# Kernel optimization log

Hardware: AMD Instinct MI355X
Metric: run time of the kernel (lower is better)

## Reference

```python
import jax, jax.numpy as jnp
import numpy as np

B, A, GS = 4, 256, 12           # graphs, atoms per graph, grid size
NG = GS ** 3                    # 1728 grid nodes per graph
K_A, K_G = 8, 32                # atom kNN, grid->atom kNN
L, CODE, HID, EDGE = 4, 64, 128, 64
NTYPES, NGAUSS, CUT, SPACING = 16, 20, 5.0, 1.5
N_NODES = B * A + B * NG


def _grid_coords():
    half = (GS - 1) * SPACING / 2.0
    g = jnp.linspace(-half, half, GS)
    mesh = jnp.meshgrid(g, g, g, indexing='ij')
    return jnp.stack(mesh, axis=-1).reshape(-1, 3)  # [NG, 3]


def _gauss_consts():
    # GaussianSmearing(type_='exp', start=0, stop=cutoff, num_gaussians=20)
    off = jnp.exp(jnp.linspace(np.log(1.0), np.log(CUT + 1.0), NGAUSS)) - 1.0
    d = jnp.diff(off)
    d = jnp.concatenate([d[:1], d])
    return off, -0.5 / d ** 2


def _build_edges(pos):
    # pos: [B*A, 3] atom coords, per-graph kNN (batch = 256 atoms per graph)
    atom_pos = pos.reshape(B, A, 3)
    # atom-atom kNN (loop=False): edge (neighbor j -> atom i)
    d2 = jnp.sum((atom_pos[:, :, None, :] - atom_pos[:, None, :, :]) ** 2, -1)
    d2 = d2 + jnp.eye(A) * 1e9  # exclude self loops
    _, nbr = jax.lax.top_k(-d2, K_A)                       # [B, A, K_A]
    src_a = (nbr + (jnp.arange(B) * A)[:, None, None]).reshape(-1)
    dst_a = jnp.repeat(jnp.arange(B * A), K_A)
    # grid->atom kNN: each grid node receives from its K_G nearest atoms
    grid = _grid_coords()
    gd2 = jnp.sum((grid[None, :, None, :] - atom_pos[:, None, :, :]) ** 2, -1)  # [B, NG, A]
    _, gn = jax.lax.top_k(-gd2, K_G)                       # [B, NG, K_G]
    src_g = (gn + (jnp.arange(B) * A)[:, None, None]).reshape(-1)
    dst_g = B * A + jnp.repeat(jnp.arange(B * NG), K_G)
    return jnp.concatenate([src_a, src_g]), jnp.concatenate([dst_a, dst_g])


def _layer(h, node_pos, src, dst, cnt, off, coeff, eW, eb, W1, b1, W2, b2, g, beta):
    rel = node_pos[src] - node_pos[dst]
    dist = jnp.clip(jnp.sqrt(jnp.sum(rel ** 2, -1)), 0.0, CUT)
    gauss = jnp.exp(coeff * (dist[:, None] - off) ** 2)    # [E, 20]
    ef = gauss @ eW + eb                                   # [E, EDGE]
    mi = jnp.concatenate([h[src], h[dst], ef], -1)         # [E, 2*CODE+EDGE]
    m = jax.nn.relu(mi @ W1 + b1) @ W2 + b2                # [E, CODE]
    aggr = jax.ops.segment_sum(m, dst, num_segments=N_NODES) / cnt[:, None]
    x = h + aggr
    mu = jnp.mean(x, -1, keepdims=True)
    var = jnp.var(x, -1, keepdims=True)
    return (x - mu) / jnp.sqrt(var + 1e-5) * g + beta


def setup_inputs() -> dict:
    key = jax.random.key(0)
    ks = jax.random.split(key, 6)
    s = 0.05
    return {
        'pos': jax.random.uniform(ks[0], (B * A, 3), minval=-8.0, maxval=8.0),
        'atom_types': jax.random.randint(ks[1], (B * A,), 0, NTYPES),
        'batch': jnp.repeat(jnp.arange(B), A),
        'edge_W': jax.random.normal(ks[2], (L, NGAUSS, EDGE)) * s,
        'edge_b': jnp.zeros((L, EDGE)),
        'W1': jax.random.normal(ks[3], (L, 2 * CODE + EDGE, HID)) * s,
        'b1': jnp.zeros((L, HID)),
        'W2': jax.random.normal(ks[4], (L, HID, CODE)) * s,
        'b2': jnp.zeros((L, CODE)),
        'ln_g': jnp.ones((L, CODE)),
        'ln_b': jnp.zeros((L, CODE)),
    }


def reference(pos, atom_types, batch, edge_W, edge_b, W1, b1, W2, b2, ln_g, ln_b):
    # node features: one-hot atoms padded to code_dim, zero grid codes
    af = jax.nn.one_hot(atom_types, NTYPES, dtype=jnp.float32)
    af = jnp.pad(af, ((0, 0), (0, CODE - NTYPES)))
    h = jnp.concatenate([af, jnp.zeros((B * NG, CODE), jnp.float32)], 0)
    node_pos = jnp.concatenate([pos, jnp.tile(_grid_coords(), (B, 1))], 0)
    src, dst = _build_edges(pos)
    cnt = jnp.clip(jax.ops.segment_sum(jnp.ones_like(dst, jnp.float32), dst,
                                       num_segments=N_NODES), 1.0)
    off, coeff = _gauss_consts()
    for l in range(L):
        h = _layer(h, node_pos, src, dst, cnt, off, coeff,
                   edge_W[l], edge_b[l], W1[l], b1[l], W2[l], b2[l],
                   ln_g[l], ln_b[l])
    return h[B * A:].reshape(B, NG, CODE)
```

## Files before the change

kernel.cpp:

```cpp
#include <hip/hip_runtime.h>
#include <hip/hip_bf16.h>
#include <math.h>

#define NATOMS 1024
#define NGRID  6912
#define NNODES 7936
#define NG_PER 1728
#define KA 8
#define KG 32
#define CODE 64
#define HID 128
#define NT 1024

typedef __hip_bfloat16 bf16;
typedef unsigned long long u64;
typedef unsigned int u32;

static void* g_buf = nullptr;
__attribute__((constructor)) static void _alloc_ws(){
  if (hipMalloc(&g_buf, (size_t)24 * 1024 * 1024) != hipSuccess) g_buf = nullptr;
}

__device__ __forceinline__ float ldf(const void* p, size_t i, int f32){
  return f32 ? ((const float*)p)[i] : __bfloat162float(((const bf16*)p)[i]);
}

__device__ __forceinline__ int ldt(const void* p, int i, int mode){
  switch(mode){
    case 1:  return ((const int*)p)[2*i];
    case 2:  return (int)((const float*)p)[i];
    case 3:  return (int)__bfloat162float(((const bf16*)p)[i]);
    default: return ((const int*)p)[i];
  }
}

__global__ void k0(const unsigned short* __restrict__ posu,
                   const unsigned short* __restrict__ typu,
                   int* __restrict__ flag, float* __restrict__ offc){
  if (blockIdx.x == 0){
    __shared__ int scnt;
    int t = threadIdx.x;
    if (t == 0) scnt = 0;
    __syncthreads();
    int c = 0;
    for (int q = 0; q < 12; q++){
      unsigned short u = posu[t + 256*q];
      int e = (u >> 7) & 0xFF;
      if (e >= 140) c++;
    }
    atomicAdd(&scnt, c);
    __syncthreads();
    if (t == 0) flag[0] = (scnt > 16) ? 1 : 0;
  } else {
    if (threadIdx.x == 0){
      int oddHigh = 0, evenHigh = 0, quadZero = 1;
      for (int k = 0; k < 16; k++){
        unsigned short o = typu[2*k+1], e = typu[2*k];
        if (o >= 0x3F00 && o <= 0x4200) oddHigh++;
        if (e >= 0x3F00 && e <= 0x4200) evenHigh++;
      }
      for (int k = 0; k < 16; k++) if (typu[4*k+2] != 0) quadZero = 0;
      int mode;
      if (oddHigh >= 8) mode = (evenHigh >= 8) ? 3 : 2;
      else              mode = quadZero ? 1 : 0;
      flag[1] = mode;
    }
    int k = (int)threadIdx.x - 64;
    if (k >= 0 && k < 20){
      double step = log(6.0) / 19.0;
      double offk = exp((double)k * step) - 1.0;
      int km = (k == 0) ? 1 : k;
      double d = (exp((double)km * step) - 1.0) - (exp((double)(km - 1) * step) - 1.0);
      offc[k]      = (float)offk;
      offc[20 + k] = (float)(-0.5 / (d * d));
    }
  }
}

__global__ void __launch_bounds__(256) k_pre(const void* __restrict__ pos,
    const void* __restrict__ types, const int* __restrict__ flag,
    float* __restrict__ node_pos, float* __restrict__ h0,
    int* __restrict__ nbrA, int* __restrict__ nbrG){
  #pragma clang fp contract(off)
  __shared__ __attribute__((aligned(16))) u64 sK[4][256];
  int f32 = flag[0];
  int b = blockIdx.x;
  int t = threadIdx.x;
  if (b < 1984){
    int tm = flag[1];
    int idx = b * 256 + t;
    if (idx < NNODES){
      if (idx < NATOMS){
        node_pos[idx*3+0] = ldf(pos, idx*3+0, f32);
        node_pos[idx*3+1] = ldf(pos, idx*3+1, f32);
        node_pos[idx*3+2] = ldf(pos, idx*3+2, f32);
      } else {
        int cell = (idx - NATOMS) % NG_PER;
        int ix = cell / 144, iy = (cell / 12) % 12, iz = cell % 12;
        node_pos[idx*3+0] = -8.25f + 1.5f * ix;
        node_pos[idx*3+1] = -8.25f + 1.5f * iy;
        node_pos[idx*3+2] = -8.25f + 1.5f * iz;
      }
    }
    int node = idx >> 6, c = idx & 63;
    float v = 0.f;
    if (node < NATOMS && c == ldt(types, node, tm)) v = 1.f;
    h0[idx] = v;
  } else if (b < 1984 + 256){
    int i = (b - 1984) * 4 + (t >> 6);
    int bb = i >> 8, li = i & 255;
    int l = t & 63;
    float px = ldf(pos,3*i,f32), py = ldf(pos,3*i+1,f32), pz = ldf(pos,3*i+2,f32);
    u64 vals[4];
    for (int q = 0; q < 4; q++){
      int c = l + 64*q;
      int j = (bb << 8) + c;
      float dx = ldf(pos,3*j+0,f32) - px;
      float dy = ldf(pos,3*j+1,f32) - py;
      float dz = ldf(pos,3*j+2,f32) - pz;
      float d2 = (dx*dx + dy*dy) + dz*dz;
      vals[q] = (c == li) ? ~0ull : (((u64)__float_as_uint(d2) << 8) | (unsigned)c);
    }
    for (int it = 0; it < KA; it++){
      u64 v = vals[0];
      for (int q = 1; q < 4; q++) if (vals[q] < v) v = vals[q];
      for (int m = 1; m < 64; m <<= 1){
        u64 ov = __shfl_xor(v, m);
        if (ov < v) v = ov;
      }
      int widx = (int)(v & 0xFF);
      if (l == 0) nbrA[i*KA + it] = (bb << 8) + widx;
      if ((widx & 63) == l) vals[widx >> 6] = ~0ull;
    }
  } else {
    int w  = t >> 6;
    int gi = (b - 2240) * 4 + w;
    int bb = gi / NG_PER, cell = gi % NG_PER;
    int ix = cell / 144, iy = (cell / 12) % 12, iz = cell % 12;
    double px = -8.25 + 1.5 * ix;
    double py = -8.25 + 1.5 * iy;
    double pz = -8.25 + 1.5 * iz;
    int l = t & 63;
    u64* sk = &sK[w][0];
    u64 vals[4];
    #pragma unroll
    for (int q = 0; q < 4; q++){
      int c = l + 64*q;
      int j = (bb << 8) + c;
      double dx = px - (double)ldf(pos,3*j+0,f32);
      double dy = py - (double)ldf(pos,3*j+1,f32);
      double dz = pz - (double)ldf(pos,3*j+2,f32);
      double d2 = dx*dx + dy*dy + dz*dz;
      u64 key = ((u64)__double_as_longlong(d2) & ~0xFFull) | (unsigned)c;
      vals[q] = key;
      sk[c] = key;
    }
    __syncthreads();
    int r0 = 0, r1 = 0, r2 = 0, r3 = 0;
    #pragma unroll 4
    for (int j = 0; j < 256; j += 2){
      ulonglong2 kk = *(const ulonglong2*)&sk[j];
      r0 += (kk.x < vals[0]); r0 += (kk.y < vals[0]);
      r1 += (kk.x < vals[1]); r1 += (kk.y < vals[1]);
      r2 += (kk.x < vals[2]); r2 += (kk.y < vals[2]);
      r3 += (kk.x < vals[3]); r3 += (kk.y < vals[3]);
    }
    int base = (bb << 8) + l;
    if (r0 < KG) nbrG[gi*KG + r0] = base;
    if (r1 < KG) nbrG[gi*KG + r1] = base + 64;
    if (r2 < KG) nbrG[gi*KG + r2] = base + 128;
    if (r3 < KG) nbrG[gi*KG + r3] = base + 192;
  }
}

__global__ void __launch_bounds__(128) k_fold(const float* __restrict__ hin,
    const void* __restrict__ W1, const void* __restrict__ b1,
    const void* __restrict__ eW, const void* __restrict__ eb,
    size_t wl, size_t b1o, size_t eWo, size_t ebo,
    const int* __restrict__ flag,
    float* __restrict__ Xd, float* __restrict__ Xs,
    float* __restrict__ Wg, float* __restrict__ b1p,
    const float* __restrict__ offc, float2* __restrict__ Tt)
{
  __shared__ __attribute__((aligned(16))) float sA[1344];
  __shared__ float sB[192];
  int f32 = flag[0];
  int t = threadIdx.x;
  int b = blockIdx.x;
  if (b < 1120){
    int isXd = (b < 992);
    size_t wo = wl + (isXd ? (size_t)64*128 : 0);
    int r0 = (isXd ? b : (b - 992)) * 8;
    float* C = isXd ? Xd : Xs;
    float w[64];
    #pragma unroll
    for (int k = 0; k < 64; k++) w[k] = ldf(W1, wo + (size_t)k*128 + t, f32);
    for (int i = t; i < 8*64; i += 128) sA[i] = hin[(size_t)r0*64 + i];
    __syncthreads();
    #pragma unroll
    for (int r = 0; r < 8; r += 4){
      float a0 = 0.f, a1 = 0.f, a2 = 0.f, a3 = 0.f;
      #pragma unroll
      for (int k4 = 0; k4 < 16; k4++){
        float4 v0 = *(const float4*)&sA[(r+0)*64 + 4*k4];
        float4 v1 = *(const float4*)&sA[(r+1)*64 + 4*k4];
        float4 v2 = *(const float4*)&sA[(r+2)*64 + 4*k4];
        float4 v3 = *(const float4*)&sA[(r+3)*64 + 4*k4];
        a0 = fmaf(v0.x, w[4*k4+0], a0); a0 = fmaf(v0.y, w[4*k4+1], a0);
        a0 = fmaf(v0.z, w[4*k4+2], a0); a0 = fmaf(v0.w, w[4*k4+3], a0);
        a1 = fmaf(v1.x, w[4*k4+0], a1); a1 = fmaf(v1.y, w[4*k4+1], a1);
        a1 = fmaf(v1.z, w[4*k4+2], a1); a1 = fmaf(v1.w, w[4*k4+3], a1);
        a2 = fmaf(v2.x, w[4*k4+0], a2); a2 = fmaf(v2.y, w[4*k4+1], a2);
        a2 = fmaf(v2.z, w[4*k4+2], a2); a2 = fmaf(v2.w, w[4*k4+3], a2);
        a3 = fmaf(v3.x, w[4*k4+0], a3); a3 = fmaf(v3.y, w[4*k4+1], a3);
        a3 = fmaf(v3.z, w[4*k4+2], a3); a3 = fmaf(v3.w, w[4*k4+3], a3);
      }
      C[(size_t)(r0 + r + 0)*128 + t] = a0;
      C[(size_t)(r0 + r + 1)*128 + t] = a1;
      C[(size_t)(r0 + r + 2)*128 + t] = a2;
      C[(size_t)(r0 + r + 3)*128 + t] = a3;
    }
  } else if (b == 1120){
    float w[64];
    #pragma unroll
    for (int k = 0; k < 64; k++) w[k] = ldf(W1, wl + (size_t)128*128 + (size_t)k*128 + t, f32);
    for (int i = t; i < 20*64; i += 128) sA[i] = ldf(eW, eWo + i, f32);
    if (t < 64) sA[1280 + t] = ldf(eb, ebo + t, f32);
    __syncthreads();
    for (int g = 0; g < 20; g++){
      float acc = 0.f;
      #pragma unroll
      for (int k4 = 0; k4 < 16; k4++){
        float4 e = *(const float4*)&sA[g*64 + 4*k4];
        acc = fmaf(e.x, w[4*k4+0], acc); acc = fmaf(e.y, w[4*k4+1], acc);
        acc = fmaf(e.z, w[4*k4+2], acc); acc = fmaf(e.w, w[4*k4+3], acc);
      }
      Wg[g*128 + t] = acc;
    }
    float acc = ldf(b1, b1o + t, f32);
    #pragma unroll
    for (int k4 = 0; k4 < 16; k4++){
      float4 e = *(const float4*)&sA[1280 + 4*k4];
      acc = fmaf(e.x, w[4*k4+0], acc); acc = fmaf(e.y, w[4*k4+1], acc);
      acc = fmaf(e.z, w[4*k4+2], acc); acc = fmaf(e.w, w[4*k4+3], acc);
    }
    b1p[t] = acc;
  } else {
    int r0 = (b - 1121) * 8;
    float w[64];
    #pragma unroll
    for (int k = 0; k < 64; k++) w[k] = ldf(W1, wl + (size_t)128*128 + (size_t)k*128 + t, f32);
    for (int i = t; i < 20*64; i += 128) sA[i] = ldf(eW, eWo + i, f32);
    for (int i = t; i < 180; i += 128){
      int row = i / 20, k = i - row*20;
      float d  = (float)(r0 + row) * (5.0f / (float)NT);
      float dd = d - offc[k];
      sB[i] = expf(offc[20 + k] * dd * dd);
    }
    __syncthreads();
    float wg[20];
    #pragma unroll
    for (int gk = 0; gk < 20; gk++){
      float acc = 0.f;
      #pragma unroll
      for (int k4 = 0; k4 < 16; k4++){
        float4 e = *(const float4*)&sA[gk*64 + 4*k4];
        acc = fmaf(e.x, w[4*k4+0], acc); acc = fmaf(e.y, w[4*k4+1], acc);
        acc = fmaf(e.z, w[4*k4+2], acc); acc = fmaf(e.w, w[4*k4+3], acc);
      }
      wg[gk] = acc;
    }
    float v[9];
    #pragma unroll
    for (int r = 0; r < 9; r++){
      float acc = 0.f;
      #pragma unroll
      for (int k = 0; k < 20; k++) acc = fmaf(sB[r*20 + k], wg[k], acc);
      v[r] = acc;
    }
    #pragma unroll
    for (int r = 0; r < 8; r++)
      Tt[(size_t)(r0 + r)*128 + t] = make_float2(v[r], v[r+1]);
  }
}

__global__ void __launch_bounds__(256) k_aggr(const float* __restrict__ Xs,
    const float* __restrict__ Xd, const int* __restrict__ nbrA,
    const int* __restrict__ nbrG, const float* __restrict__ node_pos,
    const float2* __restrict__ Tt, const float* __restrict__ b1p,
    float* __restrict__ Sbuf)
{
  __shared__ __attribute__((aligned(16))) int   sN[256];
  __shared__ __attribute__((aligned(16))) float sX[256];
  int t = threadIdx.x;
  int b = blockIdx.x;
  int KK, node0; const int* nbr;
  if (b < 32){ KK = 8;  node0 = b*32;              nbr = nbrA + b*256; }
  else       { KK = 32; node0 = NATOMS + (b-32)*8; nbr = nbrG + (size_t)(b-32)*256; }
  {
    int src = nbr[t];
    sN[t] = src;
    int node = node0 + ((b < 32) ? (t >> 3) : (t >> 5));
    float dx = node_pos[src*3+0] - node_pos[node*3+0];
    float dy = node_pos[src*3+1] - node_pos[node*3+1];
    float dz = node_pos[src*3+2] - node_pos[node*3+2];
    float dist = fminf(sqrtf(dx*dx + dy*dy + dz*dz), 5.0f);
    sX[t] = dist * ((float)NT / 5.0f);
  }
  int g = t >> 7, tt = t & 127;
  float b1v = b1p[tt];
  __syncthreads();
  float rK = 1.f / KK;
  int nLoc = (b < 32) ? 16 : 4;
  int nbase = g * nLoc;
  for (int n = 0; n < nLoc; n++){
    int node = node0 + nbase + n;
    float zb = Xd[(size_t)node*128 + tt] + b1v;
    float S = 0.f;
    int ebase = (nbase + n) * KK;
    for (int e = 0; e < KK; e += 4){
      int i0 = ebase + e;
      int4   sv = *(const int4*)&sN[i0];
      float4 xv = *(const float4*)&sX[i0];
      int ia0 = (int)xv.x; if (ia0 > NT-1) ia0 = NT-1;
      int ia1 = (int)xv.y; if (ia1 > NT-1) ia1 = NT-1;
      int ia2 = (int)xv.z; if (ia2 > NT-1) ia2 = NT-1;
      int ia3 = (int)xv.w; if (ia3 > NT-1) ia3 = NT-1;
      float f0 = xv.x - (float)ia0;
      float f1 = xv.y - (float)ia1;
      float f2 = xv.z - (float)ia2;
      float f3 = xv.w - (float)ia3;
      float2 w0 = Tt[(size_t)ia0*128 + tt];
      float2 w1 = Tt[(size_t)ia1*128 + tt];
      float2 w2 = Tt[(size_t)ia2*128 + tt];
      float2 w3 = Tt[(size_t)ia3*128 + tt];
      float a0 = zb + Xs[(size_t)sv.x*128 + tt] + fmaf(f0, w0.y - w0.x, w0.x);
      float a1 = zb + Xs[(size_t)sv.y*128 + tt] + fmaf(f1, w1.y - w1.x, w1.x);
      float a2 = zb + Xs[(size_t)sv.z*128 + tt] + fmaf(f2, w2.y - w2.x, w2.x);
      float a3 = zb + Xs[(size_t)sv.w*128 + tt] + fmaf(f3, w3.y - w3.x, w3.x);
      S += fmaxf(a0,0.f) + fmaxf(a1,0.f) + fmaxf(a2,0.f) + fmaxf(a3,0.f);
    }
    Sbuf[(size_t)node*128 + tt] = S * rK;
  }
}

__global__ void __launch_bounds__(256) k_out(const float* __restrict__ hin,
    const float* __restrict__ Sbuf,
    const void* __restrict__ W2, const void* __restrict__ b2,
    const void* __restrict__ lng, const void* __restrict__ lnb,
    size_t w2o, size_t b2o, size_t lno,
    const int* __restrict__ flag,
    float* __restrict__ hout, float* __restrict__ out, int writeOut)
{
  __shared__ float sW2[128*64];
  __shared__ __attribute__((aligned(16))) float sS[32*128];
  int f32 = flag[0];
  int t = threadIdx.x;
  int r0 = blockIdx.x * 32;
  for (int i = t; i < 128*64; i += 256) sW2[i] = ldf(W2, w2o + i, f32);
  for (int i = t; i < 32*128; i += 256) sS[i] = Sbuf[(size_t)r0*128 + i];
  int w = t >> 6, c = t & 63;
  float b2v = ldf(b2, b2o + c, f32);
  float gv  = ldf(lng, lno + c, f32);
  float bv  = ldf(lnb, lno + c, f32);
  __syncthreads();
  for (int rr = w*8; rr < w*8 + 8; rr += 2){
    float a0 = 0.f, a1 = 0.f;
    const float* s0 = &sS[rr*128];
    const float* s1 = &sS[(rr+1)*128];
    #pragma unroll
    for (int kq = 0; kq < 32; kq++){
      float4 sv0 = *(const float4*)(s0 + 4*kq);
      float4 sv1 = *(const float4*)(s1 + 4*kq);
      a0 = fmaf(sv0.x, sW2[(4*kq+0)*64+c], a0);
      a0 = fmaf(sv0.y, sW2[(4*kq+1)*64+c], a0);
      a0 = fmaf(sv0.z, sW2[(4*kq+2)*64+c], a0);
      a0 = fmaf(sv0.w, sW2[(4*kq+3)*64+c], a0);
      a1 = fmaf(sv1.x, sW2[(4*kq+0)*64+c], a1);
      a1 = fmaf(sv1.y, sW2[(4*kq+1)*64+c], a1);
      a1 = fmaf(sv1.z, sW2[(4*kq+2)*64+c], a1);
      a1 = fmaf(sv1.w, sW2[(4*kq+3)*64+c], a1);
    }
    {
      int node = r0 + rr;
      float x = hin[(size_t)node*64 + c] + a0 + b2v;
      float s = x;
      #pragma unroll
      for (int m = 1; m < 64; m <<= 1) s += __shfl_xor(s, m);
      float mu = s * (1.f/64.f);
      float d = x - mu;
      float v = d * d;
      #pragma unroll
      for (int m = 1; m < 64; m <<= 1) v += __shfl_xor(v, m);
      v *= (1.f/64.f);
      float o = d / sqrtf(v + 1e-5f) * gv + bv;
      hout[(size_t)node*64 + c] = o;
      if (writeOut && node >= NATOMS) out[(size_t)(node - NATOMS)*64 + c] = o;
    }
    {
      int node = r0 + rr + 1;
      float x = hin[(size_t)node*64 + c] + a1 + b2v;
      float s = x;
      #pragma unroll
      for (int m = 1; m < 64; m <<= 1) s += __shfl_xor(s, m);
      float mu = s * (1.f/64.f);
      float d = x - mu;
      float v = d * d;
      #pragma unroll
      for (int m = 1; m < 64; m <<= 1) v += __shfl_xor(v, m);
      v *= (1.f/64.f);
      float o = d / sqrtf(v + 1e-5f) * gv + bv;
      hout[(size_t)node*64 + c] = o;
      if (writeOut && node >= NATOMS) out[(size_t)(node - NATOMS)*64 + c] = o;
    }
  }
}

extern "C" void kernel_launch(void* const* d_in, const int* in_sizes, int n_in,
                              void* d_out, int out_size, void* d_ws, size_t ws_size,
                              hipStream_t stream) {
  const void* pos    = d_in[0];
  const void* types  = d_in[1];
  const void* edge_W = d_in[3];
  const void* edge_b = d_in[4];
  const void* W1     = d_in[5];
  const void* b1     = d_in[6];
  const void* W2     = d_in[7];
  const void* b2     = d_in[8];
  const void* lng    = d_in[9];
  const void* lnb    = d_in[10];

  const size_t NEED = (size_t)16 * 1024 * 1024;
  char* w = (ws_size >= NEED) ? (char*)d_ws : (char*)g_buf;
  if (w == nullptr) w = (char*)d_ws;

  size_t o = 0;
  auto alloc = [&](size_t bytes)->char*{
    char* r = w + o; o = (o + bytes + 255) & ~(size_t)255; return r;
  };
  float*  node_pos = (float*) alloc((size_t)NNODES*3*4);
  float*  hA       = (float*) alloc((size_t)NNODES*CODE*4);
  float*  hB       = (float*) alloc((size_t)NNODES*CODE*4);
  float*  Xs       = (float*) alloc((size_t)NATOMS*HID*4);
  float*  Xd       = (float*) alloc((size_t)NNODES*HID*4);
  float*  Sbuf     = (float*) alloc((size_t)NNODES*HID*4);
  int*    nbrA     = (int*)   alloc((size_t)NATOMS*KA*4);
  int*    nbrG     = (int*)   alloc((size_t)NGRID*KG*4);
  float*  offc     = (float*) alloc(64*4);
  float*  Wg       = (float*) alloc(20*HID*4);
  float*  b1p      = (float*) alloc(HID*4);
  int*    flag     = (int*)   alloc(64*4);
  float2* Tt       = (float2*)alloc((size_t)NT*HID*8);

  k0<<<2, 256, 0, stream>>>((const unsigned short*)pos,
                            (const unsigned short*)types, flag, offc);
  k_pre<<<3968, 256, 0, stream>>>(pos, types, flag, node_pos, hA, nbrA, nbrG);

  float* hin = hA; float* hout = hB;
  for (int l = 0; l < 4; l++){
    size_t wl  = (size_t)l*192*128;
    size_t eWo = (size_t)l*20*64, ebo = (size_t)l*64;
    size_t b1o = (size_t)l*128,   w2o = (size_t)l*128*64;
    size_t b2o = (size_t)l*64,    lno = (size_t)l*64;
    k_fold<<<1121 + 128, 128, 0, stream>>>(hin, W1, b1, edge_W, edge_b,
                                     wl, b1o, eWo, ebo, flag, Xd, Xs, Wg, b1p,
                                     offc, Tt);
    k_aggr<<<32 + NGRID/8, 256, 0, stream>>>(Xs, Xd, nbrA, nbrG, node_pos,
                                             Tt, b1p, Sbuf);
    k_out<<<NNODES/32, 256, 0, stream>>>(hin, Sbuf, W2, b2, lng, lnb,
                                         w2o, b2o, lno, flag,
                                         hout, (float*)d_out, (l == 3) ? 1 : 0);
    float* tmp = hin; hin = hout; hout = tmp;
  }
}
```

Baseline: 371.8 us.

## Remove setup kernel by detecting dtype per block and shrink k_out row tile

Drops the k0 launch by having each block of k_pre, k_fold and k_out recompute the float32/bf16 detection from pos into shared memory. The Gaussian constants are now computed inside the k_fold table blocks instead of being read from a global buffer. k_out now handles 8 rows per block instead of 32, so it launches four times as many blocks to raise parallelism. In exchange, every block does extra redundant reads of pos plus a barrier, and each k_out block reloads the full W2 matrix for fewer rows.

```diff
diff --git a/kernel.cpp b/kernel.cpp
--- a/kernel.cpp
+++ b/kernel.cpp
@@ -34,25 +34,36 @@
   }
 }
 
-__global__ void k0(const unsigned short* __restrict__ posu,
-                   const unsigned short* __restrict__ typu,
-                   int* __restrict__ flag, float* __restrict__ offc){
-  if (blockIdx.x == 0){
-    __shared__ int scnt;
-    int t = threadIdx.x;
-    if (t == 0) scnt = 0;
-    __syncthreads();
-    int c = 0;
-    for (int q = 0; q < 12; q++){
-      unsigned short u = posu[t + 256*q];
-      int e = (u >> 7) & 0xFF;
-      if (e >= 140) c++;
-    }
-    atomicAdd(&scnt, c);
-    __syncthreads();
-    if (t == 0) flag[0] = (scnt > 16) ? 1 : 0;
-  } else {
-    if (threadIdx.x == 0){
+template<int NTH>
+__device__ __forceinline__ int detect_f32(const unsigned short* __restrict__ posu,
+                                          int t, int* sflag){
+  if (t == 0) *sflag = 0;
+  __syncthreads();
+  int c = 0;
+  #pragma unroll
+  for (int q = 0; q < 3072/NTH; q++){
+    unsigned short u = posu[t + NTH*q];
+    int e = (u >> 7) & 0xFF;
+    c += (e >= 140);
+  }
+  atomicAdd(sflag, c);
+  __syncthreads();
+  return (*sflag > 16) ? 1 : 0;
+}
+
+__global__ void __launch_bounds__(256) k_pre(const void* __restrict__ pos,
+    const void* __restrict__ types,
+    float* __restrict__ node_pos, float* __restrict__ h0,
+    int* __restrict__ nbrA, int* __restrict__ nbrG){
+  #pragma clang fp contract(off)
+  __shared__ __attribute__((aligned(16))) u64 sK[4][256];
+  __shared__ int sflag[2];
+  int b = blockIdx.x;
+  int t = threadIdx.x;
+  int f32 = detect_f32<256>((const unsigned short*)pos, t, &sflag[0]);
+  if (b < 1984){
+    if (t == 0){
+      const unsigned short* typu = (const unsigned short*)types;
       int oddHigh = 0, evenHigh = 0, quadZero = 1;
       for (int k = 0; k < 16; k++){
         unsigned short o = typu[2*k+1], e = typu[2*k];
@@ -63,31 +74,10 @@
       int mode;
       if (oddHigh >= 8) mode = (evenHigh >= 8) ? 3 : 2;
       else              mode = quadZero ? 1 : 0;
-      flag[1] = mode;
-    }
-    int k = (int)threadIdx.x - 64;
-    if (k >= 0 && k < 20){
-      double step = log(6.0) / 19.0;
-      double offk = exp((double)k * step) - 1.0;
-      int km = (k == 0) ? 1 : k;
-      double d = (exp((double)km * step) - 1.0) - (exp((double)(km - 1) * step) - 1.0);
-      offc[k]      = (float)offk;
-      offc[20 + k] = (float)(-0.5 / (d * d));
-    }
-  }
-}
-
-__global__ void __launch_bounds__(256) k_pre(const void* __restrict__ pos,
-    const void* __restrict__ types, const int* __restrict__ flag,
-    float* __restrict__ node_pos, float* __restrict__ h0,
-    int* __restrict__ nbrA, int* __restrict__ nbrG){
-  #pragma clang fp contract(off)
-  __shared__ __attribute__((aligned(16))) u64 sK[4][256];
-  int f32 = flag[0];
-  int b = blockIdx.x;
-  int t = threadIdx.x;
-  if (b < 1984){
-    int tm = flag[1];
+      sflag[1] = mode;
+    }
+    __syncthreads();
+    int tm = sflag[1];
     int idx = b * 256 + t;
     if (idx < NNODES){
       if (idx < NATOMS){
@@ -177,16 +167,18 @@
     const void* __restrict__ W1, const void* __restrict__ b1,
     const void* __restrict__ eW, const void* __restrict__ eb,
     size_t wl, size_t b1o, size_t eWo, size_t ebo,
-    const int* __restrict__ flag,
+    const void* __restrict__ pos,
     float* __restrict__ Xd, float* __restrict__ Xs,
     float* __restrict__ Wg, float* __restrict__ b1p,
-    const float* __restrict__ offc, float2* __restrict__ Tt)
+    float2* __restrict__ Tt)
 {
   __shared__ __attribute__((aligned(16))) float sA[1344];
   __shared__ float sB[192];
-  int f32 = flag[0];
+  __shared__ float sOff[40];
+  __shared__ int sflag;
   int t = threadIdx.x;
   int b = blockIdx.x;
+  int f32 = detect_f32<128>((const unsigned short*)pos, t, &sflag);
   if (b < 1120){
     int isXd = (b < 992);
     size_t wo = wl + (isXd ? (size_t)64*128 : 0);
@@ -247,15 +239,24 @@
     b1p[t] = acc;
   } else {
     int r0 = (b - 1121) * 8;
+    if (t < 20){
+      double step = log(6.0) / 19.0;
+      double offk = exp((double)t * step) - 1.0;
+      int km = (t == 0) ? 1 : t;
+      double d = (exp((double)km * step) - 1.0) - (exp((double)(km - 1) * step) - 1.0);
+      sOff[t]      = (float)offk;
+      sOff[20 + t] = (float)(-0.5 / (d * d));
+    }
     float w[64];
     #pragma unroll
     for (int k = 0; k < 64; k++) w[k] = ldf(W1, wl + (size_t)128*128 + (size_t)k*128 + t, f32);
     for (int i = t; i < 20*64; i += 128) sA[i] = ldf(eW, eWo + i, f32);
+    __syncthreads();
     for (int i = t; i < 180; i += 128){
       int row = i / 20, k = i - row*20;
       float d  = (float)(r0 + row) * (5.0f / (float)NT);
-      float dd = d - offc[k];
-      sB[i] = expf(offc[20 + k] * dd * dd);
+      float dd = d - sOff[k];
+      sB[i] = expf(sOff[20 + k] * dd * dd);
     }
     __syncthreads();
     float wg[20];
@@ -349,22 +350,24 @@
     const void* __restrict__ W2, const void* __restrict__ b2,
     const void* __restrict__ lng, const void* __restrict__ lnb,
     size_t w2o, size_t b2o, size_t lno,
-    const int* __restrict__ flag,
+    const void* __restrict__ pos,
     float* __restrict__ hout, float* __restrict__ out, int writeOut)
 {
   __shared__ float sW2[128*64];
-  __shared__ __attribute__((aligned(16))) float sS[32*128];
-  int f32 = flag[0];
+  __shared__ __attribute__((aligned(16))) float sS[8*128];
+  __shared__ int sflag;
   int t = threadIdx.x;
-  int r0 = blockIdx.x * 32;
+  int f32 = detect_f32<256>((const unsigned short*)pos, t, &sflag);
+  int r0 = blockIdx.x * 8;
   for (int i = t; i < 128*64; i += 256) sW2[i] = ldf(W2, w2o + i, f32);
-  for (int i = t; i < 32*128; i += 256) sS[i] = Sbuf[(size_t)r0*128 + i];
+  for (int i = t; i < 8*128; i += 256) sS[i] = Sbuf[(size_t)r0*128 + i];
   int w = t >> 6, c = t & 63;
   float b2v = ldf(b2, b2o + c, f32);
   float gv  = ldf(lng, lno + c, f32);
   float bv  = ldf(lnb, lno + c, f32);
   __syncthreads();
-  for (int rr = w*8; rr < w*8 + 8; rr += 2){
+  int rr = w * 2;
+  {
     float a0 = 0.f, a1 = 0.f;
     const float* s0 = &sS[rr*128];
     const float* s1 = &sS[(rr+1)*128];
@@ -446,15 +449,11 @@
   float*  Sbuf     = (float*) alloc((size_t)NNODES*HID*4);
   int*    nbrA     = (int*)   alloc((size_t)NATOMS*KA*4);
   int*    nbrG     = (int*)   alloc((size_t)NGRID*KG*4);
-  float*  offc     = (float*) alloc(64*4);
   float*  Wg       = (float*) alloc(20*HID*4);
   float*  b1p      = (float*) alloc(HID*4);
-  int*    flag     = (int*)   alloc(64*4);
   float2* Tt       = (float2*)alloc((size_t)NT*HID*8);
 
-  k0<<<2, 256, 0, stream>>>((const unsigned short*)pos,
-                            (const unsigned short*)types, flag, offc);
-  k_pre<<<3968, 256, 0, stream>>>(pos, types, flag, node_pos, hA, nbrA, nbrG);
+  k_pre<<<3968, 256, 0, stream>>>(pos, types, node_pos, hA, nbrA, nbrG);
 
   float* hin = hA; float* hout = hB;
   for (int l = 0; l < 4; l++){
@@ -463,13 +462,13 @@
     size_t b1o = (size_t)l*128,   w2o = (size_t)l*128*64;
     size_t b2o = (size_t)l*64,    lno = (size_t)l*64;
     k_fold<<<1121 + 128, 128, 0, stream>>>(hin, W1, b1, edge_W, edge_b,
-                                     wl, b1o, eWo, ebo, flag, Xd, Xs, Wg, b1p,
-                                     offc, Tt);
+                                     wl, b1o, eWo, ebo, pos, Xd, Xs, Wg, b1p,
+                                     Tt);
     k_aggr<<<32 + NGRID/8, 256, 0, stream>>>(Xs, Xd, nbrA, nbrG, node_pos,
                                              Tt, b1p, Sbuf);
-    k_out<<<NNODES/32, 256, 0, stream>>>(hin, Sbuf, W2, b2, lng, lnb,
-                                         w2o, b2o, lno, flag,
-                                         hout, (float*)d_out, (l == 3) ? 1 : 0);
+    k_out<<<NNODES/8, 256, 0, stream>>>(hin, Sbuf, W2, b2, lng, lnb,
+                                        w2o, b2o, lno, pos,
+                                        hout, (float*)d_out, (l == 3) ? 1 : 0);
     float* tmp = hin; hin = hout; hout = tmp;
   }
 }
```

New measurement: 477.8 us. 1.29x slower.

## Hoist per-layer edge tables into k_pre and fuse next-layer fold into output kernel

Applied to the files above, without the earlier changes.

The edge-distance lookup table (Tt), folded gaussian weights (Wg) and bias (b1p) for all four layers are now computed once in extra blocks of the preprocessing kernel instead of in each layer's fold kernel. The Xs/Xd projections of the next layer are computed inside the output/layernorm kernel from the freshly normalized rows kept in shared memory. This removes three k_fold launches and a reread of h from global memory. In exchange the output kernel uses more shared memory and registers, which may lower occupancy, and the workspace grows to hold per-layer tables.

```diff
diff --git a/kernel.cpp b/kernel.cpp
--- a/kernel.cpp
+++ b/kernel.cpp
@@ -80,9 +80,15 @@
 __global__ void __launch_bounds__(256) k_pre(const void* __restrict__ pos,
     const void* __restrict__ types, const int* __restrict__ flag,
     float* __restrict__ node_pos, float* __restrict__ h0,
-    int* __restrict__ nbrA, int* __restrict__ nbrG){
+    int* __restrict__ nbrA, int* __restrict__ nbrG,
+    const void* __restrict__ W1, const void* __restrict__ b1,
+    const void* __restrict__ eW, const void* __restrict__ eb,
+    const float* __restrict__ offc,
+    float* __restrict__ Wg, float* __restrict__ b1p, float2* __restrict__ Tt){
   #pragma clang fp contract(off)
   __shared__ __attribute__((aligned(16))) u64 sK[4][256];
+  __shared__ __attribute__((aligned(16))) float sA[1344];
+  __shared__ float sB[192];
   int f32 = flag[0];
   int b = blockIdx.x;
   int t = threadIdx.x;
@@ -132,7 +138,7 @@
       if (l == 0) nbrA[i*KA + it] = (bb << 8) + widx;
       if ((widx & 63) == l) vals[widx >> 6] = ~0ull;
     }
-  } else {
+  } else if (b < 3968){
     int w  = t >> 6;
     int gi = (b - 2240) * 4 + w;
     int bb = gi / NG_PER, cell = gi % NG_PER;
@@ -170,117 +176,120 @@
     if (r1 < KG) nbrG[gi*KG + r1] = base + 64;
     if (r2 < KG) nbrG[gi*KG + r2] = base + 128;
     if (r3 < KG) nbrG[gi*KG + r3] = base + 192;
+  } else {
+    int wb = b - 3968;
+    int layer = wb / 129, sub = wb - layer * 129;
+    size_t wl  = (size_t)layer*192*128;
+    size_t eWo = (size_t)layer*20*64, ebo = (size_t)layer*64;
+    size_t b1o = (size_t)layer*128;
+    if (sub == 0){
+      for (int i = t; i < 20*64; i += 256) sA[i] = ldf(eW, eWo + i, f32);
+      if (t < 64) sA[1280 + t] = ldf(eb, ebo + t, f32);
+      __syncthreads();
+      if (t < 128){
+        float w[64];
+        #pragma unroll
+        for (int k = 0; k < 64; k++) w[k] = ldf(W1, wl + (size_t)128*128 + (size_t)k*128 + t, f32);
+        for (int g = 0; g < 20; g++){
+          float acc = 0.f;
+          #pragma unroll
+          for (int k4 = 0; k4 < 16; k4++){
+            float4 e = *(const float4*)&sA[g*64 + 4*k4];
+            acc = fmaf(e.x, w[4*k4+0], acc); acc = fmaf(e.y, w[4*k4+1], acc);
+            acc = fmaf(e.z, w[4*k4+2], acc); acc = fmaf(e.w, w[4*k4+3], acc);
+          }
+          Wg[layer*20*128 + g*128 + t] = acc;
+        }
+        float acc = ldf(b1, b1o + t, f32);
+        #pragma unroll
+        for (int k4 = 0; k4 < 16; k4++){
+          float4 e = *(const float4*)&sA[1280 + 4*k4];
+          acc = fmaf(e.x, w[4*k4+0], acc); acc = fmaf(e.y, w[4*k4+1], acc);
+          acc = fmaf(e.z, w[4*k4+2], acc); acc = fmaf(e.w, w[4*k4+3], acc);
+        }
+        b1p[layer*128 + t] = acc;
+      }
+    } else {
+      int r0 = (sub - 1) * 8;
+      for (int i = t; i < 20*64; i += 256) sA[i] = ldf(eW, eWo + i, f32);
+      for (int i = t; i < 180; i += 256){
+        int row = i / 20, k = i - row*20;
+        float d  = (float)(r0 + row) * (5.0f / (float)NT);
+        float dd = d - offc[k];
+        sB[i] = expf(offc[20 + k] * dd * dd);
+      }
+      __syncthreads();
+      if (t < 128){
+        float w[64];
+        #pragma unroll
+        for (int k = 0; k < 64; k++) w[k] = ldf(W1, wl + (size_t)128*128 + (size_t)k*128 + t, f32);
+        float wg[20];
+        #pragma unroll
+        for (int gk = 0; gk < 20; gk++){
+          float acc = 0.f;
+          #pragma unroll
+          for (int k4 = 0; k4 < 16; k4++){
+            float4 e = *(const float4*)&sA[gk*64 + 4*k4];
+            acc = fmaf(e.x, w[4*k4+0], acc); acc = fmaf(e.y, w[4*k4+1], acc);
+            acc = fmaf(e.z, w[4*k4+2], acc); acc = fmaf(e.w, w[4*k4+3], acc);
+          }
+          wg[gk] = acc;
+        }
+        float v[9];
+        #pragma unroll
+        for (int r = 0; r < 9; r++){
+          float acc = 0.f;
+          #pragma unroll
+          for (int k = 0; k < 20; k++) acc = fmaf(sB[r*20 + k], wg[k], acc);
+          v[r] = acc;
+        }
+        #pragma unroll
+        for (int r = 0; r < 8; r++)
+          Tt[(size_t)layer*NT*128 + (size_t)(r0 + r)*128 + t] = make_float2(v[r], v[r+1]);
+      }
+    }
   }
 }
 
 __global__ void __launch_bounds__(128) k_fold(const float* __restrict__ hin,
-    const void* __restrict__ W1, const void* __restrict__ b1,
-    const void* __restrict__ eW, const void* __restrict__ eb,
-    size_t wl, size_t b1o, size_t eWo, size_t ebo,
-    const int* __restrict__ flag,
-    float* __restrict__ Xd, float* __restrict__ Xs,
-    float* __restrict__ Wg, float* __restrict__ b1p,
-    const float* __restrict__ offc, float2* __restrict__ Tt)
+    const void* __restrict__ W1, size_t wl, const int* __restrict__ flag,
+    float* __restrict__ Xd, float* __restrict__ Xs)
 {
-  __shared__ __attribute__((aligned(16))) float sA[1344];
-  __shared__ float sB[192];
+  __shared__ __attribute__((aligned(16))) float sA[512];
   int f32 = flag[0];
   int t = threadIdx.x;
   int b = blockIdx.x;
-  if (b < 1120){
-    int isXd = (b < 992);
-    size_t wo = wl + (isXd ? (size_t)64*128 : 0);
-    int r0 = (isXd ? b : (b - 992)) * 8;
-    float* C = isXd ? Xd : Xs;
-    float w[64];
-    #pragma unroll
-    for (int k = 0; k < 64; k++) w[k] = ldf(W1, wo + (size_t)k*128 + t, f32);
-    for (int i = t; i < 8*64; i += 128) sA[i] = hin[(size_t)r0*64 + i];
-    __syncthreads();
-    #pragma unroll
-    for (int r = 0; r < 8; r += 4){
-      float a0 = 0.f, a1 = 0.f, a2 = 0.f, a3 = 0.f;
-      #pragma unroll
-      for (int k4 = 0; k4 < 16; k4++){
-        float4 v0 = *(const float4*)&sA[(r+0)*64 + 4*k4];
-        float4 v1 = *(const float4*)&sA[(r+1)*64 + 4*k4];
-        float4 v2 = *(const float4*)&sA[(r+2)*64 + 4*k4];
-        float4 v3 = *(const float4*)&sA[(r+3)*64 + 4*k4];
-        a0 = fmaf(v0.x, w[4*k4+0], a0); a0 = fmaf(v0.y, w[4*k4+1], a0);
-        a0 = fmaf(v0.z, w[4*k4+2], a0); a0 = fmaf(v0.w, w[4*k4+3], a0);
-        a1 = fmaf(v1.x, w[4*k4+0], a1); a1 = fmaf(v1.y, w[4*k4+1], a1);
-        a1 = fmaf(v1.z, w[4*k4+2], a1); a1 = fmaf(v1.w, w[4*k4+3], a1);
-        a2 = fmaf(v2.x, w[4*k4+0], a2); a2 = fmaf(v2.y, w[4*k4+1], a2);
-        a2 = fmaf(v2.z, w[4*k4+2], a2); a2 = fmaf(v2.w, w[4*k4+3], a2);
-        a3 = fmaf(v3.x, w[4*k4+0], a3); a3 = fmaf(v3.y, w[4*k4+1], a3);
-        a3 = fmaf(v3.z, w[4*k4+2], a3); a3 = fmaf(v3.w, w[4*k4+3], a3);
-      }
-      C[(size_t)(r0 + r + 0)*128 + t] = a0;
-      C[(size_t)(r0 + r + 1)*128 + t] = a1;
-      C[(size_t)(r0 + r + 2)*128 + t] = a2;
-      C[(size_t)(r0 + r + 3)*128 + t] = a3;
-    }
-  } else if (b == 1120){
-    float w[64];
-    #pragma unroll
-    for (int k = 0; k < 64; k++) w[k] = ldf(W1, wl + (size_t)128*128 + (size_t)k*128 + t, f32);
-    for (int i = t; i < 20*64; i += 128) sA[i] = ldf(eW, eWo + i, f32);
-    if (t < 64) sA[1280 + t] = ldf(eb, ebo + t, f32);
-    __syncthreads();
-    for (int g = 0; g < 20; g++){
-      float acc = 0.f;
-      #pragma unroll
-      for (int k4 = 0; k4 < 16; k4++){
-        float4 e = *(const float4*)&sA[g*64 + 4*k4];
-        acc = fmaf(e.x, w[4*k4+0], acc); acc = fmaf(e.y, w[4*k4+1], acc);
-        acc = fmaf(e.z, w[4*k4+2], acc); acc = fmaf(e.w, w[4*k4+3], acc);
-      }
-      Wg[g*128 + t] = acc;
-    }
-    float acc = ldf(b1, b1o + t, f32);
+  int isXd = (b < 992);
+  size_t wo = wl + (isXd ? (size_t)64*128 : 0);
+  int r0 = (isXd ? b : (b - 992)) * 8;
+  float* C = isXd ? Xd : Xs;
+  float w[64];
+  #pragma unroll
+  for (int k = 0; k < 64; k++) w[k] = ldf(W1, wo + (size_t)k*128 + t, f32);
+  for (int i = t; i < 8*64; i += 128) sA[i] = hin[(size_t)r0*64 + i];
+  __syncthreads();
+  #pragma unroll
+  for (int r = 0; r < 8; r += 4){
+    float a0 = 0.f, a1 = 0.f, a2 = 0.f, a3 = 0.f;
     #pragma unroll
     for (int k4 = 0; k4 < 16; k4++){
-      float4 e = *(const float4*)&sA[1280 + 4*k4];
-      acc = fmaf(e.x, w[4*k4+0], acc); acc = fmaf(e.y, w[4*k4+1], acc);
-      acc = fmaf(e.z, w[4*k4+2], acc); acc = fmaf(e.w, w[4*k4+3], acc);
-    }
-    b1p[t] = acc;
-  } else {
-    int r0 = (b - 1121) * 8;
-    float w[64];
-    #pragma unroll
-    for (int k = 0; k < 64; k++) w[k] = ldf(W1, wl + (size_t)128*128 + (size_t)k*128 + t, f32);
-    for (int i = t; i < 20*64; i += 128) sA[i] = ldf(eW, eWo + i, f32);
-    for (int i = t; i < 180; i += 128){
-      int row = i / 20, k = i - row*20;
-      float d  = (float)(r0 + row) * (5.0f / (float)NT);
-      float dd = d - offc[k];
-      sB[i] = expf(offc[20 + k] * dd * dd);
-    }
-    __syncthreads();
-    float wg[20];
-    #pragma unroll
-    for (int gk = 0; gk < 20; gk++){
-      float acc = 0.f;
-      #pragma unroll
-      for (int k4 = 0; k4 < 16; k4++){
-        float4 e = *(const float4*)&sA[gk*64 + 4*k4];
-        acc = fmaf(e.x, w[4*k4+0], acc); acc = fmaf(e.y, w[4*k4+1], acc);
-        acc = fmaf(e.z, w[4*k4+2], acc); acc = fmaf(e.w, w[4*k4+3], acc);
-      }
-      wg[gk] = acc;
-    }
-    float v[9];
-    #pragma unroll
-    for (int r = 0; r < 9; r++){
-      float acc = 0.f;
-      #pragma unroll
-      for (int k = 0; k < 20; k++) acc = fmaf(sB[r*20 + k], wg[k], acc);
-      v[r] = acc;
-    }
-    #pragma unroll
-    for (int r = 0; r < 8; r++)
-      Tt[(size_t)(r0 + r)*128 + t] = make_float2(v[r], v[r+1]);
+      float4 v0 = *(const float4*)&sA[(r+0)*64 + 4*k4];
+      float4 v1 = *(const float4*)&sA[(r+1)*64 + 4*k4];
+      float4 v2 = *(const float4*)&sA[(r+2)*64 + 4*k4];
+      float4 v3 = *(const float4*)&sA[(r+3)*64 + 4*k4];
+      a0 = fmaf(v0.x, w[4*k4+0], a0); a0 = fmaf(v0.y, w[4*k4+1], a0);
+      a0 = fmaf(v0.z, w[4*k4+2], a0); a0 = fmaf(v0.w, w[4*k4+3], a0);
+      a1 = fmaf(v1.x, w[4*k4+0], a1); a1 = fmaf(v1.y, w[4*k4+1], a1);
+      a1 = fmaf(v1.z, w[4*k4+2], a1); a1 = fmaf(v1.w, w[4*k4+3], a1);
+      a2 = fmaf(v2.x, w[4*k4+0], a2); a2 = fmaf(v2.y, w[4*k4+1], a2);
+      a2 = fmaf(v2.z, w[4*k4+2], a2); a2 = fmaf(v2.w, w[4*k4+3], a2);
+      a3 = fmaf(v3.x, w[4*k4+0], a3); a3 = fmaf(v3.y, w[4*k4+1], a3);
+      a3 = fmaf(v3.z, w[4*k4+2], a3); a3 = fmaf(v3.w, w[4*k4+3], a3);
+    }
+    C[(size_t)(r0 + r + 0)*128 + t] = a0;
+    C[(size_t)(r0 + r + 1)*128 + t] = a1;
+    C[(size_t)(r0 + r + 2)*128 + t] = a2;
+    C[(size_t)(r0 + r + 3)*128 + t] = a3;
   }
 }
 
@@ -344,16 +353,19 @@
   }
 }
 
-__global__ void __launch_bounds__(256) k_out(const float* __restrict__ hin,
+__global__ void __launch_bounds__(256) k_outfold(const float* __restrict__ hin,
     const float* __restrict__ Sbuf,
     const void* __restrict__ W2, const void* __restrict__ b2,
     const void* __restrict__ lng, const void* __restrict__ lnb,
     size_t w2o, size_t b2o, size_t lno,
+    const void* __restrict__ W1, size_t wlNext, int doFold,
     const int* __restrict__ flag,
+    float* __restrict__ Xd, float* __restrict__ Xs,
     float* __restrict__ hout, float* __restrict__ out, int writeOut)
 {
   __shared__ float sW2[128*64];
   __shared__ __attribute__((aligned(16))) float sS[32*128];
+  __shared__ __attribute__((aligned(16))) float sH[32*64];
   int f32 = flag[0];
   int t = threadIdx.x;
   int r0 = blockIdx.x * 32;
@@ -395,6 +407,7 @@
       v *= (1.f/64.f);
       float o = d / sqrtf(v + 1e-5f) * gv + bv;
       hout[(size_t)node*64 + c] = o;
+      sH[rr*64 + c] = o;
       if (writeOut && node >= NATOMS) out[(size_t)(node - NATOMS)*64 + c] = o;
     }
     {
@@ -411,7 +424,68 @@
       v *= (1.f/64.f);
       float o = d / sqrtf(v + 1e-5f) * gv + bv;
       hout[(size_t)node*64 + c] = o;
+      sH[(rr+1)*64 + c] = o;
       if (writeOut && node >= NATOMS) out[(size_t)(node - NATOMS)*64 + c] = o;
+    }
+  }
+  if (!doFold) return;
+  __syncthreads();
+  int col = t & 127, half = t >> 7;
+  int rbase = half * 16;
+  {
+    float w1r[64];
+    #pragma unroll
+    for (int k = 0; k < 64; k++)
+      w1r[k] = ldf(W1, wlNext + (size_t)64*128 + (size_t)k*128 + col, f32);
+    for (int r = rbase; r < rbase + 16; r += 4){
+      float a0 = 0.f, a1 = 0.f, a2 = 0.f, a3 = 0.f;
+      #pragma unroll
+      for (int k4 = 0; k4 < 16; k4++){
+        float4 v0 = *(const float4*)&sH[(r+0)*64 + 4*k4];
+        float4 v1 = *(const float4*)&sH[(r+1)*64 + 4*k4];
+        float4 v2 = *(const float4*)&sH[(r+2)*64 + 4*k4];
+        float4 v3 = *(const float4*)&sH[(r+3)*64 + 4*k4];
+        a0 = fmaf(v0.x, w1r[4*k4+0], a0); a0 = fmaf(v0.y, w1r[4*k4+1], a0);
+        a0 = fmaf(v0.z, w1r[4*k4+2], a0); a0 = fmaf(v0.w, w1r[4*k4+3], a0);
+        a1 = fmaf(v1.x, w1r[4*k4+0], a1); a1 = fmaf(v1.y, w1r[4*k4+1], a1);
+        a1 = fmaf(v1.z, w1r[4*k4+2], a1); a1 = fmaf(v1.w, w1r[4*k4+3], a1);
+        a2 = fmaf(v2.x, w1r[4*k4+0], a2); a2 = fmaf(v2.y, w1r[4*k4+1], a2);
+        a2 = fmaf(v2.z, w1r[4*k4+2], a2); a2 = fmaf(v2.w, w1r[4*k4+3], a2);
+        a3 = fmaf(v3.x, w1r[4*k4+0], a3); a3 = fmaf(v3.y, w1r[4*k4+1], a3);
+        a3 = fmaf(v3.z, w1r[4*k4+2], a3); a3 = fmaf(v3.w, w1r[4*k4+3], a3);
+      }
+      Xd[(size_t)(r0 + r + 0)*128 + col] = a0;
+      Xd[(size_t)(r0 + r + 1)*128 + col] = a1;
+      Xd[(size_t)(r0 + r + 2)*128 + col] = a2;
+      Xd[(size_t)(r0 + r + 3)*128 + col] = a3;
+    }
+  }
+  if (blockIdx.x < 32){
+    float w1r[64];
+    #pragma unroll
+    for (int k = 0; k < 64; k++)
+      w1r[k] = ldf(W1, wlNext + (size_t)k*128 + col, f32);
+    for (int r = rbase; r < rbase + 16; r += 4){
+      float a0 = 0.f, a1 = 0.f, a2 = 0.f, a3 = 0.f;
+      #pragma unroll
+      for (int k4 = 0; k4 < 16; k4++){
+        float4 v0 = *(const float4*)&sH[(r+0)*64 + 4*k4];
+        float4 v1 = *(const float4*)&sH[(r+1)*64 + 4*k4];
+        float4 v2 = *(const float4*)&sH[(r+2)*64 + 4*k4];
+        float4 v3 = *(const float4*)&sH[(r+3)*64 + 4*k4];
+        a0 = fmaf(v0.x, w1r[4*k4+0], a0); a0 = fmaf(v0.y, w1r[4*k4+1], a0);
+        a0 = fmaf(v0.z, w1r[4*k4+2], a0); a0 = fmaf(v0.w, w1r[4*k4+3], a0);
+        a1 = fmaf(v1.x, w1r[4*k4+0], a1); a1 = fmaf(v1.y, w1r[4*k4+1], a1);
+        a1 = fmaf(v1.z, w1r[4*k4+2], a1); a1 = fmaf(v1.w, w1r[4*k4+3], a1);
+        a2 = fmaf(v2.x, w1r[4*k4+0], a2); a2 = fmaf(v2.y, w1r[4*k4+1], a2);
+        a2 = fmaf(v2.z, w1r[4*k4+2], a2); a2 = fmaf(v2.w, w1r[4*k4+3], a2);
+        a3 = fmaf(v3.x, w1r[4*k4+0], a3); a3 = fmaf(v3.y, w1r[4*k4+1], a3);
+        a3 = fmaf(v3.z, w1r[4*k4+2], a3); a3 = fmaf(v3.w, w1r[4*k4+3], a3);
+      }
+      Xs[(size_t)(r0 + r + 0)*128 + col] = a0;
+      Xs[(size_t)(r0 + r + 1)*128 + col] = a1;
+      Xs[(size_t)(r0 + r + 2)*128 + col] = a2;
+      Xs[(size_t)(r0 + r + 3)*128 + col] = a3;
     }
   }
 }
@@ -430,7 +504,7 @@
   const void* lng    = d_in[9];
   const void* lnb    = d_in[10];
 
-  const size_t NEED = (size_t)16 * 1024 * 1024;
+  const size_t NEED = (size_t)20 * 1024 * 1024;
   char* w = (ws_size >= NEED) ? (char*)d_ws : (char*)g_buf;
   if (w == nullptr) w = (char*)d_ws;
 
@@ -447,29 +521,31 @@
   int*    nbrA     = (int*)   alloc((size_t)NATOMS*KA*4);
   int*    nbrG     = (int*)   alloc((size_t)NGRID*KG*4);
   float*  offc     = (float*) alloc(64*4);
-  float*  Wg       = (float*) alloc(20*HID*4);
-  float*  b1p      = (float*) alloc(HID*4);
+  float*  Wg       = (float*) alloc((size_t)4*20*HID*4);
+  float*  b1p      = (float*) alloc((size_t)4*HID*4);
   int*    flag     = (int*)   alloc(64*4);
-  float2* Tt       = (float2*)alloc((size_t)NT*HID*8);
+  float2* Tt       = (float2*)alloc((size_t)4*NT*HID*8);
 
   k0<<<2, 256, 0, stream>>>((const unsigned short*)pos,
                             (const unsigned short*)types, flag, offc);
-  k_pre<<<3968, 256, 0, stream>>>(pos, types, flag, node_pos, hA, nbrA, nbrG);
+  k_pre<<<3968 + 4*129, 256, 0, stream>>>(pos, types, flag, node_pos, hA,
+                                          nbrA, nbrG, W1, b1, edge_W, edge_b,
+                                          offc, Wg, b1p, Tt);
+  k_fold<<<1120, 128, 0, stream>>>(hA, W1, (size_t)0, flag, Xd, Xs);
 
   float* hin = hA; float* hout = hB;
   for (int l = 0; l < 4; l++){
-    size_t wl  = (size_t)l*192*128;
-    size_t eWo = (size_t)l*20*64, ebo = (size_t)l*64;
-    size_t b1o = (size_t)l*128,   w2o = (size_t)l*128*64;
-    size_t b2o = (size_t)l*64,    lno = (size_t)l*64;
-    k_fold<<<1121 + 128, 128, 0, stream>>>(hin, W1, b1, edge_W, edge_b,
-                                     wl, b1o, eWo, ebo, flag, Xd, Xs, Wg, b1p,
-                                     offc, Tt);
+    size_t w2o = (size_t)l*128*64;
+    size_t b2o = (size_t)l*64, lno = (size_t)l*64;
+    size_t wlN = (size_t)(l+1)*192*128;
     k_aggr<<<32 + NGRID/8, 256, 0, stream>>>(Xs, Xd, nbrA, nbrG, node_pos,
-                                             Tt, b1p, Sbuf);
-    k_out<<<NNODES/32, 256, 0, stream>>>(hin, Sbuf, W2, b2, lng, lnb,
-                                         w2o, b2o, lno, flag,
-                                         hout, (float*)d_out, (l == 3) ? 1 : 0);
+                                             Tt + (size_t)l*NT*HID, b1p + l*HID,
+                                             Sbuf);
+    k_outfold<<<NNODES/32, 256, 0, stream>>>(hin, Sbuf, W2, b2, lng, lnb,
+                                             w2o, b2o, lno,
+                                             W1, wlN, (l < 3) ? 1 : 0,
+                                             flag, Xd, Xs,
+                                             hout, (float*)d_out, (l == 3) ? 1 : 0);
     float* tmp = hin; hin = hout; hout = tmp;
   }
 }
```

New measurement: 367.8 us. No clear change (-1.1%).
